# Optimization experiments

Hardware: AMD Instinct MI355X
Metric: run time of the kernel (lower is better)

Reference implementation:

```python
import jax, jax.numpy as jnp
import numpy as np

H, B, S, D, T = 4, 16, 2048, 128, 5  # n_head, batch, seq_len, d_model, num event types
BAND_K = 64  # latest-k band width, as in get_latest_k_mask


def setup_inputs() -> dict:
    key = jax.random.key(0)
    ks = jax.random.split(key, 5)
    output = jax.random.normal(ks[0], (B, S, D), dtype=jnp.float32)
    # banded 'latest-k' mask: mask[i, i:i+k] = 1  (start=max(i,i-k+1)=i, end=min(S,i+k))
    i = jnp.arange(S)
    band = ((i[None, :] >= i[:, None]) & (i[None, :] < i[:, None] + BAND_K)).astype(jnp.float32)
    local_cor = band[None]  # [1, S, S]
    cor_matrix = jax.random.normal(ks[1], (T, D), dtype=jnp.float32)
    event_type = jax.random.randint(ks[2], (B, S), 1, T + 1)  # 1-based event ids in [1, T]
    # per-head linear3 params (xavier-ish); self.linear is unused in forward
    W3 = jax.random.normal(ks[3], (H, D, D), dtype=jnp.float32) / np.sqrt(D)
    b3 = jnp.zeros((H, D), dtype=jnp.float32)
    return dict(output=output, local_cor=local_cor, cor_matrix=cor_matrix,
                event_type=event_type, W3=W3, b3=b3)


def reference(output, local_cor, cor_matrix, event_type, W3, b3):
    # (corr^T @ cor_matrix[et-1]).mean(2) == einsum('bsd,bs->bd', corr, cor_matrix[et-1].mean(-1))
    g = cor_matrix.mean(-1)[event_type - 1]  # [B, S]
    x = output
    sum_seq = jnp.zeros_like(output)          # sum over heads of [B,S,D]
    sum_head = jnp.zeros((output.shape[0], output.shape[2]), output.dtype)  # [B,D]
    for h in range(H):
        z = jax.nn.elu(jnp.einsum('bsd,ed->bse', x, W3[h]) + b3[h])  # linear3 + ELU
        corr = jnp.matmul(local_cor, z)       # [1,S,S] @ [B,S,D] -> [B,S,D]
        head_out = jnp.einsum('bsd,bs->bd', corr, g)  # [B,D]
        sum_seq = sum_seq + corr
        sum_head = sum_head + head_out
        x = corr                               # next head consumes correlation_output
    return (sum_seq, sum_head)
```

## Files before the change

kernel.cpp:

```cpp
#include <hip/hip_runtime.h>
#include <math.h>

#define NHEAD 4
#define BATCH 16
#define SEQ   2048
#define DMODEL 128
#define NTYPES 5
#define BAND  64
#define MROWS (BATCH * SEQ)

typedef __attribute__((ext_vector_type(8))) short bf16x8;
typedef __attribute__((ext_vector_type(4))) float f32x4;
typedef __attribute__((ext_vector_type(4))) unsigned int u32x4;

static __device__ __forceinline__ unsigned short f2bf(float f) {
  unsigned int u = __float_as_uint(f);
  unsigned int r = (u + 0x7fffu + ((u >> 16) & 1u)) >> 16;
  return (unsigned short)r;
}
static __device__ __forceinline__ float bflo(unsigned int v) {
  return __uint_as_float(v << 16);
}
static __device__ __forceinline__ float bfhi(unsigned int v) {
  return __uint_as_float(v & 0xffff0000u);
}
static __device__ __forceinline__ unsigned int pkbf(float lo, float hi) {
  return ((unsigned int)f2bf(hi) << 16) | (unsigned int)f2bf(lo);
}
static __device__ __forceinline__ int xcd_swz(int blk, int nwg) {
  return (blk & 7) * (nwg >> 3) + (blk >> 3);
}

__global__ __launch_bounds__(256) void init_kernel(
    const float* __restrict__ corm,
    const int* __restrict__ et,
    const float* __restrict__ W3,
    unsigned short* __restrict__ wbf,
    float* __restrict__ gbuf,
    float* __restrict__ sum_head) {
  __shared__ float rowmean[NTYPES];
  const int tid = threadIdx.x;
  const long t = (long)blockIdx.x * 256 + tid;

  if (t < (NHEAD * DMODEL * DMODEL) / 8) {
    const long u = t * 8;
    float4 a = *reinterpret_cast<const float4*>(W3 + u);
    float4 b = *reinterpret_cast<const float4*>(W3 + u + 4);
    unsigned short o[8];
    o[0] = f2bf(a.x); o[1] = f2bf(a.y); o[2] = f2bf(a.z); o[3] = f2bf(a.w);
    o[4] = f2bf(b.x); o[5] = f2bf(b.y); o[6] = f2bf(b.z); o[7] = f2bf(b.w);
    *reinterpret_cast<u32x4*>(wbf + u) = *reinterpret_cast<u32x4*>(o);
  }
  if (tid < NTYPES) {
    float s = 0.f;
    for (int d = 0; d < DMODEL; ++d) s += corm[tid * DMODEL + d];
    rowmean[tid] = s * (1.0f / DMODEL);
  }
  __syncthreads();
  if (t < MROWS) gbuf[t] = rowmean[et[t] - 1];
  if (t < BATCH * DMODEL) sum_head[t] = 0.f;
}

__global__ __launch_bounds__(512, 4) void gemm0_kernel(
    const float* __restrict__ X0,
    const unsigned short* __restrict__ Wb,
    const float* __restrict__ bvec,
    unsigned short* __restrict__ Zb) {
  __shared__ __align__(16) char lds[64 * 272 + 128 * 272];
  char* Xl = lds;
  char* Wl = lds + 64 * 272;
  const int tid = threadIdx.x;
  const int swz = xcd_swz(blockIdx.x, gridDim.x);
  const int row0 = swz * 64;

  #pragma unroll
  for (int it = 0; it < 2; ++it) {
    const int u = it * 512 + tid;
    const int r = u >> 4, g4 = u & 15;
    const float* xs = X0 + (long)(row0 + r) * DMODEL + g4 * 8;
    float4 f0 = *reinterpret_cast<const float4*>(xs);
    float4 f1 = *reinterpret_cast<const float4*>(xs + 4);
    unsigned short o[8];
    o[0] = f2bf(f0.x); o[1] = f2bf(f0.y); o[2] = f2bf(f0.z); o[3] = f2bf(f0.w);
    o[4] = f2bf(f1.x); o[5] = f2bf(f1.y); o[6] = f2bf(f1.z); o[7] = f2bf(f1.w);
    *reinterpret_cast<u32x4*>(Xl + r * 272 + g4 * 16) = *reinterpret_cast<u32x4*>(o);
  }
  #pragma unroll
  for (int it = 0; it < 4; ++it) {
    const int u = it * 512 + tid;
    const int e = u >> 4, g4 = u & 15;
    u32x4 v = *reinterpret_cast<const u32x4*>(Wb + e * DMODEL + g4 * 8);
    *reinterpret_cast<u32x4*>(Wl + e * 272 + g4 * 16) = v;
  }
  __syncthreads();

  const int wv = tid >> 6, l = tid & 63;
  const int mv = wv >> 1, nh = wv & 1;
  const int lr = l & 15, lk = l >> 4;
  f32x4 acc[4];
  #pragma unroll
  for (int n = 0; n < 4; ++n) acc[n] = (f32x4){0.f, 0.f, 0.f, 0.f};
  #pragma unroll
  for (int t = 0; t < 4; ++t) {
    const bf16x8 a = *reinterpret_cast<const bf16x8*>(
        Xl + (mv * 16 + lr) * 272 + (t * 4 + lk) * 16);
    #pragma unroll
    for (int n = 0; n < 4; ++n) {
      const bf16x8 bfrag = *reinterpret_cast<const bf16x8*>(
          Wl + (nh * 64 + n * 16 + lr) * 272 + (t * 4 + lk) * 16);
      acc[n] = __builtin_amdgcn_mfma_f32_16x16x32_bf16(a, bfrag, acc[n], 0, 0, 0);
    }
  }
  #pragma unroll
  for (int n = 0; n < 4; ++n) {
    const int col = nh * 64 + n * 16 + lr;
    const float bias = bvec[col];
    #pragma unroll
    for (int r = 0; r < 4; ++r) {
      const int row = row0 + mv * 16 + lk * 4 + r;
      float v = acc[n][r] + bias;
      const float e = expm1f(fminf(v, 0.f));
      v = v > 0.f ? v : e;
      Zb[(long)row * DMODEL + col] = f2bf(v);
    }
  }
}

template <int ACC>
__global__ __launch_bounds__(512, 4) void fused_band_gemm(
    const unsigned short* __restrict__ Zin,
    const unsigned short* __restrict__ CSin,
    unsigned short* __restrict__ Cout,
    const unsigned short* __restrict__ Wb,
    const float* __restrict__ bvec,
    unsigned short* __restrict__ Zout,
    float* __restrict__ SH,
    const float* __restrict__ Gbuf) {
  __shared__ __align__(16) char lds[56320];
  char* Xl = lds;
  float2* s8 = reinterpret_cast<float2*>(lds);
  unsigned int* zl = reinterpret_cast<unsigned int*>(lds + 17408);
  char* Wl = lds + 17408;
  float* hred = reinterpret_cast<float*>(lds + 52224);

  const int tid = threadIdx.x;
  const int swz = xcd_swz(blockIdx.x, gridDim.x);
  const int r0 = swz * 64;
  const int b = r0 >> 11, s0 = r0 & 2047;

  const unsigned int* zsrc = reinterpret_cast<const unsigned int*>(Zin) +
                             (long)b * SEQ * 64;
  #pragma unroll
  for (int it = 0; it < 4; ++it) {
    const int u = it * 512 + tid;
    const int r = u >> 4, c4 = u & 15;
    const int s = s0 + r;
    u32x4 v = (u32x4){0u, 0u, 0u, 0u};
    if (s < SEQ) v = *reinterpret_cast<const u32x4*>(zsrc + (long)s * 64 + c4 * 4);
    *reinterpret_cast<u32x4*>(zl + r * 64 + c4 * 4) = v;
  }

  const int p = tid & 63, q = tid >> 6;

  unsigned int csr[8];
  if (ACC) {
    #pragma unroll
    for (int i = 0; i < 8; ++i)
      csr[i] = *reinterpret_cast<const unsigned int*>(
          CSin + ((long)r0 + q * 8 + i) * DMODEL + 2 * p);
  }
  __syncthreads();

  #pragma unroll
  for (int j = 0; j < 2; ++j) {
    const int k = q * 2 + j;
    float a0 = 0.f, a1 = 0.f;
    #pragma unroll
    for (int jr = 0; jr < 8; ++jr) {
      const unsigned int v = zl[(k * 8 + jr) * 64 + p];
      a0 += bflo(v); a1 += bfhi(v);
    }
    s8[k * 64 + p] = make_float2(a0, a1);
  }
  __syncthreads();

  float w0 = 0.f, w1 = 0.f;
  #pragma unroll
  for (int j = 0; j < 8; ++j) {
    const float2 v = s8[(q + j) * 64 + p];
    w0 += v.x; w1 += v.y;
  }
  __syncthreads();

  float hs0 = 0.f, hs1 = 0.f;
  const float* gr = Gbuf + (long)b * SEQ + s0;
  #pragma unroll
  for (int i = 0; i < 8; ++i) {
    const int s = q * 8 + i;
    const float c0v = w0, c1v = w1;
    const float g = gr[s];
    hs0 += c0v * g; hs1 += c1v * g;
    unsigned int pk;
    if (ACC)
      pk = pkbf(c0v + bflo(csr[i]), c1v + bfhi(csr[i]));
    else
      pk = pkbf(c0v, c1v);
    *reinterpret_cast<unsigned int*>(
        Cout + ((long)r0 + s) * DMODEL + 2 * p) = pk;
    *reinterpret_cast<unsigned int*>(Xl + s * 272 + p * 4) =
        ACC ? pkbf(c0v, c1v) : pk;
    const unsigned int va = zl[(s + BAND) * 64 + p];
    const unsigned int vs = zl[s * 64 + p];
    w0 += bflo(va) - bflo(vs);
    w1 += bfhi(va) - bfhi(vs);
  }
  *reinterpret_cast<float2*>(hred + (p * 8 + q) * 2) = make_float2(hs0, hs1);
  __syncthreads();

  if (q == 0) {
    float t0 = 0.f, t1 = 0.f;
    #pragma unroll
    for (int k = 0; k < 8; ++k) {
      const float2 v = *reinterpret_cast<const float2*>(hred + (p * 8 + k) * 2);
      t0 += v.x; t1 += v.y;
    }
    atomicAdd(SH + b * DMODEL + 2 * p, t0);
    atomicAdd(SH + b * DMODEL + 2 * p + 1, t1);
  }
  #pragma unroll
  for (int it = 0; it < 4; ++it) {
    const int u = it * 512 + tid;
    const int e = u >> 4, g4 = u & 15;
    u32x4 v = *reinterpret_cast<const u32x4*>(Wb + e * DMODEL + g4 * 8);
    *reinterpret_cast<u32x4*>(Wl + e * 272 + g4 * 16) = v;
  }
  __syncthreads();

  const int wv = tid >> 6, l = tid & 63;
  const int mv = wv >> 1, nh = wv & 1;
  const int lr = l & 15, lk = l >> 4;
  f32x4 acc[4];
  #pragma unroll
  for (int n = 0; n < 4; ++n) acc[n] = (f32x4){0.f, 0.f, 0.f, 0.f};
  #pragma unroll
  for (int t = 0; t < 4; ++t) {
    const bf16x8 a = *reinterpret_cast<const bf16x8*>(
        Xl + (mv * 16 + lr) * 272 + (t * 4 + lk) * 16);
    #pragma unroll
    for (int n = 0; n < 4; ++n) {
      const bf16x8 bfrag = *reinterpret_cast<const bf16x8*>(
          Wl + (nh * 64 + n * 16 + lr) * 272 + (t * 4 + lk) * 16);
      acc[n] = __builtin_amdgcn_mfma_f32_16x16x32_bf16(a, bfrag, acc[n], 0, 0, 0);
    }
  }
  #pragma unroll
  for (int n = 0; n < 4; ++n) {
    const int col = nh * 64 + n * 16 + lr;
    const float bias = bvec[col];
    #pragma unroll
    for (int r = 0; r < 4; ++r) {
      const int row = r0 + mv * 16 + lk * 4 + r;
      float v = acc[n][r] + bias;
      const float e = expm1f(fminf(v, 0.f));
      v = v > 0.f ? v : e;
      Zout[(long)row * DMODEL + col] = f2bf(v);
    }
  }
}

__global__ __launch_bounds__(512, 4) void band3_kernel(
    const unsigned short* __restrict__ Zin,
    const unsigned short* __restrict__ CSin,
    float* __restrict__ SS,
    float* __restrict__ SH,
    const float* __restrict__ Gbuf) {
  __shared__ __align__(16) char lds[45056];
  unsigned int* zl = reinterpret_cast<unsigned int*>(lds);
  float2* s8 = reinterpret_cast<float2*>(lds + 32768);
  float* hred = reinterpret_cast<float*>(lds + 40960);

  const int tid = threadIdx.x;
  const int swz = xcd_swz(blockIdx.x, gridDim.x);
  const int r0 = swz * 64;
  const int b = r0 >> 11, s0 = r0 & 2047;

  const unsigned int* zsrc = reinterpret_cast<const unsigned int*>(Zin) +
                             (long)b * SEQ * 64;
  #pragma unroll
  for (int it = 0; it < 4; ++it) {
    const int u = it * 512 + tid;
    const int r = u >> 4, c4 = u & 15;
    const int s = s0 + r;
    u32x4 v = (u32x4){0u, 0u, 0u, 0u};
    if (s < SEQ) v = *reinterpret_cast<const u32x4*>(zsrc + (long)s * 64 + c4 * 4);
    *reinterpret_cast<u32x4*>(zl + r * 64 + c4 * 4) = v;
  }

  const int p = tid & 63, q = tid >> 6;
  unsigned int csr[8];
  #pragma unroll
  for (int i = 0; i < 8; ++i)
    csr[i] = *reinterpret_cast<const unsigned int*>(
        CSin + ((long)r0 + q * 8 + i) * DMODEL + 2 * p);
  __syncthreads();

  #pragma unroll
  for (int j = 0; j < 2; ++j) {
    const int k = q * 2 + j;
    float a0 = 0.f, a1 = 0.f;
    #pragma unroll
    for (int jr = 0; jr < 8; ++jr) {
      const unsigned int v = zl[(k * 8 + jr) * 64 + p];
      a0 += bflo(v); a1 += bfhi(v);
    }
    s8[k * 64 + p] = make_float2(a0, a1);
  }
  __syncthreads();

  float w0 = 0.f, w1 = 0.f;
  #pragma unroll
  for (int j = 0; j < 8; ++j) {
    const float2 v = s8[(q + j) * 64 + p];
    w0 += v.x; w1 += v.y;
  }
  float hs0 = 0.f, hs1 = 0.f;
  const float* gr = Gbuf + (long)b * SEQ + s0;
  #pragma unroll
  for (int i = 0; i < 8; ++i) {
    const int s = q * 8 + i;
    const float c0v = w0, c1v = w1;
    const float g = gr[s];
    hs0 += c0v * g; hs1 += c1v * g;
    const long orow = ((long)r0 + s) * DMODEL + 2 * p;
    float2 o;
    o.x = c0v + bflo(csr[i]);
    o.y = c1v + bfhi(csr[i]);
    *reinterpret_cast<float2*>(SS + orow) = o;
    const unsigned int va = zl[(s + BAND) * 64 + p];
    const unsigned int vs = zl[s * 64 + p];
    w0 += bflo(va) - bflo(vs);
    w1 += bfhi(va) - bfhi(vs);
  }
  *reinterpret_cast<float2*>(hred + (p * 8 + q) * 2) = make_float2(hs0, hs1);
  __syncthreads();
  if (q == 0) {
    float t0 = 0.f, t1 = 0.f;
    #pragma unroll
    for (int k = 0; k < 8; ++k) {
      const float2 v = *reinterpret_cast<const float2*>(hred + (p * 8 + k) * 2);
      t0 += v.x; t1 += v.y;
    }
    atomicAdd(SH + b * DMODEL + 2 * p, t0);
    atomicAdd(SH + b * DMODEL + 2 * p + 1, t1);
  }
}

extern "C" void kernel_launch(void* const* d_in, const int* in_sizes, int n_in,
                              void* d_out, int out_size, void* d_ws, size_t ws_size,
                              hipStream_t stream) {
  const float* x0   = (const float*)d_in[0];
  const float* corm = (const float*)d_in[2];
  const int*   et   = (const int*)d_in[3];
  const float* W3   = (const float*)d_in[4];
  const float* b3   = (const float*)d_in[5];

  float* out_ss = (float*)d_out;
  float* out_sh = out_ss + (size_t)MROWS * DMODEL;

  char* ws = (char*)d_ws;
  const size_t MB = 1024 * 1024;
  unsigned short* A = (unsigned short*)(ws + 0 * MB);
  unsigned short* B = (unsigned short*)(ws + 8 * MB);
  unsigned short* C = (unsigned short*)(ws + 16 * MB);
  unsigned short* D = (unsigned short*)(ws + 24 * MB);
  unsigned short* E = (unsigned short*)(ws + 32 * MB);
  unsigned short* wbf  = (unsigned short*)(ws + 40 * MB);
  float*          gbuf = (float*)(ws + 40 * MB + 131072);

  const size_t WSTR = (size_t)DMODEL * DMODEL;

  init_kernel<<<128, 256, 0, stream>>>(corm, et, W3, wbf, gbuf, out_sh);
  gemm0_kernel<<<512, 512, 0, stream>>>(x0, wbf, b3, A);
  fused_band_gemm<0><<<512, 512, 0, stream>>>(
      A, nullptr, B, wbf + 1 * WSTR, b3 + 1 * DMODEL, E, out_sh, gbuf);
  fused_band_gemm<1><<<512, 512, 0, stream>>>(
      E, B, C, wbf + 2 * WSTR, b3 + 2 * DMODEL, A, out_sh, gbuf);
  fused_band_gemm<1><<<512, 512, 0, stream>>>(
      A, C, D, wbf + 3 * WSTR, b3 + 3 * DMODEL, E, out_sh, gbuf);
  band3_kernel<<<512, 512, 0, stream>>>(E, D, out_ss, out_sh, gbuf);
}
```

Baseline: 63.17 us.

## Drop init kernel and fuse last band-gemm stage with final band pass

Removes the separate init kernel. Weight bf16 conversion, the event-type gate lookup and the zeroing of sum_head now happen inside the consuming kernels. The last fused band-GEMM and the final band kernel are merged into one 1024-thread block kernel. That block computes the head-2 band sum, the head-3 GEMM+ELU in LDS and the head-3 band sum, and writes the fp32 outputs directly, so the D/E intermediate round trips and two launches go away. In exchange, every block redundantly converts weights and recomputes row means, and the new kernel uses about 140KB of LDS, which limits occupancy to one block per CU.

```diff
diff --git a/kernel.cpp b/kernel.cpp
--- a/kernel.cpp
+++ b/kernel.cpp
@@ -31,47 +31,20 @@
   return (blk & 7) * (nwg >> 3) + (blk >> 3);
 }
 
-__global__ __launch_bounds__(256) void init_kernel(
-    const float* __restrict__ corm,
-    const int* __restrict__ et,
-    const float* __restrict__ W3,
-    unsigned short* __restrict__ wbf,
-    float* __restrict__ gbuf,
-    float* __restrict__ sum_head) {
-  __shared__ float rowmean[NTYPES];
-  const int tid = threadIdx.x;
-  const long t = (long)blockIdx.x * 256 + tid;
-
-  if (t < (NHEAD * DMODEL * DMODEL) / 8) {
-    const long u = t * 8;
-    float4 a = *reinterpret_cast<const float4*>(W3 + u);
-    float4 b = *reinterpret_cast<const float4*>(W3 + u + 4);
-    unsigned short o[8];
-    o[0] = f2bf(a.x); o[1] = f2bf(a.y); o[2] = f2bf(a.z); o[3] = f2bf(a.w);
-    o[4] = f2bf(b.x); o[5] = f2bf(b.y); o[6] = f2bf(b.z); o[7] = f2bf(b.w);
-    *reinterpret_cast<u32x4*>(wbf + u) = *reinterpret_cast<u32x4*>(o);
-  }
-  if (tid < NTYPES) {
-    float s = 0.f;
-    for (int d = 0; d < DMODEL; ++d) s += corm[tid * DMODEL + d];
-    rowmean[tid] = s * (1.0f / DMODEL);
-  }
-  __syncthreads();
-  if (t < MROWS) gbuf[t] = rowmean[et[t] - 1];
-  if (t < BATCH * DMODEL) sum_head[t] = 0.f;
-}
-
 __global__ __launch_bounds__(512, 4) void gemm0_kernel(
     const float* __restrict__ X0,
-    const unsigned short* __restrict__ Wb,
+    const float* __restrict__ W3h,
     const float* __restrict__ bvec,
-    unsigned short* __restrict__ Zb) {
+    unsigned short* __restrict__ Zb,
+    float* __restrict__ SH) {
   __shared__ __align__(16) char lds[64 * 272 + 128 * 272];
   char* Xl = lds;
   char* Wl = lds + 64 * 272;
   const int tid = threadIdx.x;
   const int swz = xcd_swz(blockIdx.x, gridDim.x);
   const int row0 = swz * 64;
+
+  if (blockIdx.x < 16 && tid < DMODEL) SH[blockIdx.x * DMODEL + tid] = 0.f;
 
   #pragma unroll
   for (int it = 0; it < 2; ++it) {
@@ -89,8 +62,13 @@
   for (int it = 0; it < 4; ++it) {
     const int u = it * 512 + tid;
     const int e = u >> 4, g4 = u & 15;
-    u32x4 v = *reinterpret_cast<const u32x4*>(Wb + e * DMODEL + g4 * 8);
-    *reinterpret_cast<u32x4*>(Wl + e * 272 + g4 * 16) = v;
+    const float* wsrc = W3h + e * DMODEL + g4 * 8;
+    float4 f0 = *reinterpret_cast<const float4*>(wsrc);
+    float4 f1 = *reinterpret_cast<const float4*>(wsrc + 4);
+    unsigned short o[8];
+    o[0] = f2bf(f0.x); o[1] = f2bf(f0.y); o[2] = f2bf(f0.z); o[3] = f2bf(f0.w);
+    o[4] = f2bf(f1.x); o[5] = f2bf(f1.y); o[6] = f2bf(f1.z); o[7] = f2bf(f1.w);
+    *reinterpret_cast<u32x4*>(Wl + e * 272 + g4 * 16) = *reinterpret_cast<u32x4*>(o);
   }
   __syncthreads();
 
@@ -131,12 +109,15 @@
     const unsigned short* __restrict__ Zin,
     const unsigned short* __restrict__ CSin,
     unsigned short* __restrict__ Cout,
-    const unsigned short* __restrict__ Wb,
+    const float* __restrict__ W3h,
     const float* __restrict__ bvec,
     unsigned short* __restrict__ Zout,
     float* __restrict__ SH,
-    const float* __restrict__ Gbuf) {
+    const int* __restrict__ et,
+    const float* __restrict__ corm) {
   __shared__ __align__(16) char lds[56320];
+  __shared__ float g_lds[64];
+  __shared__ float rowmean[NTYPES];
   char* Xl = lds;
   float2* s8 = reinterpret_cast<float2*>(lds);
   unsigned int* zl = reinterpret_cast<unsigned int*>(lds + 17408);
@@ -159,9 +140,12 @@
     if (s < SEQ) v = *reinterpret_cast<const u32x4*>(zsrc + (long)s * 64 + c4 * 4);
     *reinterpret_cast<u32x4*>(zl + r * 64 + c4 * 4) = v;
   }
-
+  if (tid < NTYPES) {
+    float s = 0.f;
+    for (int d = 0; d < DMODEL; ++d) s += corm[tid * DMODEL + d];
+    rowmean[tid] = s * (1.0f / DMODEL);
+  }
   const int p = tid & 63, q = tid >> 6;
-
   unsigned int csr[8];
   if (ACC) {
     #pragma unroll
@@ -171,6 +155,7 @@
   }
   __syncthreads();
 
+  if (tid < 64) g_lds[tid] = rowmean[et[(long)b * SEQ + s0 + tid] - 1];
   #pragma unroll
   for (int j = 0; j < 2; ++j) {
     const int k = q * 2 + j;
@@ -193,20 +178,18 @@
   __syncthreads();
 
   float hs0 = 0.f, hs1 = 0.f;
-  const float* gr = Gbuf + (long)b * SEQ + s0;
   #pragma unroll
   for (int i = 0; i < 8; ++i) {
     const int s = q * 8 + i;
     const float c0v = w0, c1v = w1;
-    const float g = gr[s];
+    const float g = g_lds[s];
     hs0 += c0v * g; hs1 += c1v * g;
     unsigned int pk;
     if (ACC)
       pk = pkbf(c0v + bflo(csr[i]), c1v + bfhi(csr[i]));
     else
       pk = pkbf(c0v, c1v);
-    *reinterpret_cast<unsigned int*>(
-        Cout + ((long)r0 + s) * DMODEL + 2 * p) = pk;
+    *reinterpret_cast<unsigned int*>(Cout + ((long)r0 + s) * DMODEL + 2 * p) = pk;
     *reinterpret_cast<unsigned int*>(Xl + s * 272 + p * 4) =
         ACC ? pkbf(c0v, c1v) : pk;
     const unsigned int va = zl[(s + BAND) * 64 + p];
@@ -231,8 +214,13 @@
   for (int it = 0; it < 4; ++it) {
     const int u = it * 512 + tid;
     const int e = u >> 4, g4 = u & 15;
-    u32x4 v = *reinterpret_cast<const u32x4*>(Wb + e * DMODEL + g4 * 8);
-    *reinterpret_cast<u32x4*>(Wl + e * 272 + g4 * 16) = v;
+    const float* wsrc = W3h + e * DMODEL + g4 * 8;
+    float4 f0 = *reinterpret_cast<const float4*>(wsrc);
+    float4 f1 = *reinterpret_cast<const float4*>(wsrc + 4);
+    unsigned short o[8];
+    o[0] = f2bf(f0.x); o[1] = f2bf(f0.y); o[2] = f2bf(f0.z); o[3] = f2bf(f0.w);
+    o[4] = f2bf(f1.x); o[5] = f2bf(f1.y); o[6] = f2bf(f1.z); o[7] = f2bf(f1.w);
+    *reinterpret_cast<u32x4*>(Wl + e * 272 + g4 * 16) = *reinterpret_cast<u32x4*>(o);
   }
   __syncthreads();
 
@@ -268,52 +256,85 @@
   }
 }
 
-__global__ __launch_bounds__(512, 4) void band3_kernel(
+__global__ __launch_bounds__(1024) void f2final_kernel(
     const unsigned short* __restrict__ Zin,
     const unsigned short* __restrict__ CSin,
+    const float* __restrict__ W3h,
+    const float* __restrict__ bvec,
     float* __restrict__ SS,
     float* __restrict__ SH,
-    const float* __restrict__ Gbuf) {
-  __shared__ __align__(16) char lds[45056];
-  unsigned int* zl = reinterpret_cast<unsigned int*>(lds);
-  float2* s8 = reinterpret_cast<float2*>(lds + 32768);
-  float* hred = reinterpret_cast<float*>(lds + 40960);
+    const int* __restrict__ et,
+    const float* __restrict__ corm) {
+  __shared__ __align__(16) char lds[140032];
+  __shared__ float g_lds[64];
+  __shared__ float rowmean[NTYPES];
+  unsigned int* zst = reinterpret_cast<unsigned int*>(lds);
+  char* Xl = lds + 49920;
+  char* Wl = lds + 84736;
+  float2* s8 = reinterpret_cast<float2*>(lds + 119552);
+  float* hred = reinterpret_cast<float*>(lds + 131840);
 
   const int tid = threadIdx.x;
   const int swz = xcd_swz(blockIdx.x, gridDim.x);
   const int r0 = swz * 64;
   const int b = r0 >> 11, s0 = r0 & 2047;
+  const int p = tid & 63, q = tid >> 6;
 
   const unsigned int* zsrc = reinterpret_cast<const unsigned int*>(Zin) +
                              (long)b * SEQ * 64;
   #pragma unroll
-  for (int it = 0; it < 4; ++it) {
-    const int u = it * 512 + tid;
+  for (int it = 0; it < 3; ++it) {
+    const int u = it * 1024 + tid;
     const int r = u >> 4, c4 = u & 15;
     const int s = s0 + r;
     u32x4 v = (u32x4){0u, 0u, 0u, 0u};
     if (s < SEQ) v = *reinterpret_cast<const u32x4*>(zsrc + (long)s * 64 + c4 * 4);
-    *reinterpret_cast<u32x4*>(zl + r * 64 + c4 * 4) = v;
-  }
-
-  const int p = tid & 63, q = tid >> 6;
+    *reinterpret_cast<u32x4*>(zst + r * 65 + c4 * 4) = v;
+  }
+  #pragma unroll
+  for (int it = 0; it < 2; ++it) {
+    const int u = it * 1024 + tid;
+    const int e = u >> 4, g4 = u & 15;
+    const float* wsrc = W3h + e * DMODEL + g4 * 8;
+    float4 f0 = *reinterpret_cast<const float4*>(wsrc);
+    float4 f1 = *reinterpret_cast<const float4*>(wsrc + 4);
+    unsigned short o[8];
+    o[0] = f2bf(f0.x); o[1] = f2bf(f0.y); o[2] = f2bf(f0.z); o[3] = f2bf(f0.w);
+    o[4] = f2bf(f1.x); o[5] = f2bf(f1.y); o[6] = f2bf(f1.z); o[7] = f2bf(f1.w);
+    *reinterpret_cast<u32x4*>(Wl + e * 272 + g4 * 16) = *reinterpret_cast<u32x4*>(o);
+  }
+  if (tid < NTYPES) {
+    float s = 0.f;
+    for (int d = 0; d < DMODEL; ++d) s += corm[tid * DMODEL + d];
+    rowmean[tid] = s * (1.0f / DMODEL);
+  }
   unsigned int csr[8];
-  #pragma unroll
-  for (int i = 0; i < 8; ++i)
-    csr[i] = *reinterpret_cast<const unsigned int*>(
-        CSin + ((long)r0 + q * 8 + i) * DMODEL + 2 * p);
-  __syncthreads();
-
-  #pragma unroll
-  for (int j = 0; j < 2; ++j) {
-    const int k = q * 2 + j;
+  if (q < 8) {
+    #pragma unroll
+    for (int i = 0; i < 8; ++i)
+      csr[i] = *reinterpret_cast<const unsigned int*>(
+          CSin + ((long)r0 + q * 8 + i) * DMODEL + 2 * p);
+  }
+  __syncthreads();
+
+  if (tid < 64) g_lds[tid] = rowmean[et[(long)b * SEQ + s0 + tid] - 1];
+  {
     float a0 = 0.f, a1 = 0.f;
     #pragma unroll
     for (int jr = 0; jr < 8; ++jr) {
-      const unsigned int v = zl[(k * 8 + jr) * 64 + p];
+      const unsigned int v = zst[(q * 8 + jr) * 65 + p];
       a0 += bflo(v); a1 += bfhi(v);
     }
-    s8[k * 64 + p] = make_float2(a0, a1);
+    s8[q * 64 + p] = make_float2(a0, a1);
+    if (q < 8) {
+      float b0 = 0.f, b1 = 0.f;
+      #pragma unroll
+      for (int jr = 0; jr < 8; ++jr) {
+        const unsigned int v = zst[((16 + q) * 8 + jr) * 65 + p];
+        b0 += bflo(v); b1 += bfhi(v);
+      }
+      s8[(16 + q) * 64 + p] = make_float2(b0, b1);
+    }
   }
   __syncthreads();
 
@@ -324,30 +345,103 @@
     w0 += v.x; w1 += v.y;
   }
   float hs0 = 0.f, hs1 = 0.f;
-  const float* gr = Gbuf + (long)b * SEQ + s0;
   #pragma unroll
   for (int i = 0; i < 8; ++i) {
     const int s = q * 8 + i;
     const float c0v = w0, c1v = w1;
-    const float g = gr[s];
-    hs0 += c0v * g; hs1 += c1v * g;
-    const long orow = ((long)r0 + s) * DMODEL + 2 * p;
-    float2 o;
-    o.x = c0v + bflo(csr[i]);
-    o.y = c1v + bfhi(csr[i]);
-    *reinterpret_cast<float2*>(SS + orow) = o;
-    const unsigned int va = zl[(s + BAND) * 64 + p];
-    const unsigned int vs = zl[s * 64 + p];
+    if (q < 8) {
+      const float g = g_lds[s];
+      hs0 += c0v * g; hs1 += c1v * g;
+    }
+    *reinterpret_cast<unsigned int*>(Xl + s * 272 + p * 4) = pkbf(c0v, c1v);
+    const unsigned int va = zst[(s + BAND) * 65 + p];
+    const unsigned int vs = zst[s * 65 + p];
     w0 += bflo(va) - bflo(vs);
     w1 += bfhi(va) - bfhi(vs);
   }
-  *reinterpret_cast<float2*>(hred + (p * 8 + q) * 2) = make_float2(hs0, hs1);
+  __syncthreads();
+
+  {
+    const int l = tid & 63;
+    const int mv = q >> 1, nh = q & 1;
+    const int lr = l & 15, lk = l >> 4;
+    f32x4 acc[4];
+    #pragma unroll
+    for (int n = 0; n < 4; ++n) acc[n] = (f32x4){0.f, 0.f, 0.f, 0.f};
+    #pragma unroll
+    for (int t = 0; t < 4; ++t) {
+      const bf16x8 a = *reinterpret_cast<const bf16x8*>(
+          Xl + (mv * 16 + lr) * 272 + (t * 4 + lk) * 16);
+      #pragma unroll
+      for (int n = 0; n < 4; ++n) {
+        const bf16x8 bfrag = *reinterpret_cast<const bf16x8*>(
+            Wl + (nh * 64 + n * 16 + lr) * 272 + (t * 4 + lk) * 16);
+        acc[n] = __builtin_amdgcn_mfma_f32_16x16x32_bf16(a, bfrag, acc[n], 0, 0, 0);
+      }
+    }
+    #pragma unroll
+    for (int n = 0; n < 4; ++n) {
+      const int col = nh * 64 + n * 16 + lr;
+      const float bias = bvec[col];
+      #pragma unroll
+      for (int r = 0; r < 4; ++r) {
+        const int row = mv * 16 + lk * 4 + r;
+        float v = acc[n][r] + bias;
+        const float e = expm1f(fminf(v, 0.f));
+        v = v > 0.f ? v : e;
+        const unsigned short bz =
+            (s0 + row < SEQ) ? f2bf(v) : (unsigned short)0;
+        *reinterpret_cast<unsigned short*>(
+            reinterpret_cast<char*>(zst) + row * 260 + col * 2) = bz;
+      }
+    }
+  }
+  __syncthreads();
+
+  {
+    float a0 = 0.f, a1 = 0.f;
+    #pragma unroll
+    for (int jr = 0; jr < 8; ++jr) {
+      const unsigned int v = zst[(q * 8 + jr) * 65 + p];
+      a0 += bflo(v); a1 += bfhi(v);
+    }
+    s8[q * 64 + p] = make_float2(a0, a1);
+  }
+  __syncthreads();
+
+  if (q < 8) {
+    float v0 = 0.f, v1 = 0.f;
+    #pragma unroll
+    for (int j = 0; j < 8; ++j) {
+      const float2 v = s8[(q + j) * 64 + p];
+      v0 += v.x; v1 += v.y;
+    }
+    #pragma unroll
+    for (int i = 0; i < 8; ++i) {
+      const int s = q * 8 + i;
+      const float c3l = v0, c3h = v1;
+      const float g = g_lds[s];
+      hs0 += c3l * g; hs1 += c3h * g;
+      const unsigned int c2 =
+          *reinterpret_cast<const unsigned int*>(Xl + s * 272 + p * 4);
+      float2 o;
+      o.x = c3l + bflo(c2) + bflo(csr[i]);
+      o.y = c3h + bfhi(c2) + bfhi(csr[i]);
+      *reinterpret_cast<float2*>(SS + ((long)r0 + s) * DMODEL + 2 * p) = o;
+      const unsigned int va = zst[(s + BAND) * 65 + p];
+      const unsigned int vs = zst[s * 65 + p];
+      v0 += bflo(va) - bflo(vs);
+      v1 += bfhi(va) - bfhi(vs);
+    }
+  }
+
+  *reinterpret_cast<float2*>(hred + (p * 16 + q) * 2) = make_float2(hs0, hs1);
   __syncthreads();
   if (q == 0) {
     float t0 = 0.f, t1 = 0.f;
     #pragma unroll
-    for (int k = 0; k < 8; ++k) {
-      const float2 v = *reinterpret_cast<const float2*>(hred + (p * 8 + k) * 2);
+    for (int k = 0; k < 16; ++k) {
+      const float2 v = *reinterpret_cast<const float2*>(hred + (p * 16 + k) * 2);
       t0 += v.x; t1 += v.y;
     }
     atomicAdd(SH + b * DMODEL + 2 * p, t0);
@@ -372,20 +466,15 @@
   unsigned short* A = (unsigned short*)(ws + 0 * MB);
   unsigned short* B = (unsigned short*)(ws + 8 * MB);
   unsigned short* C = (unsigned short*)(ws + 16 * MB);
-  unsigned short* D = (unsigned short*)(ws + 24 * MB);
-  unsigned short* E = (unsigned short*)(ws + 32 * MB);
-  unsigned short* wbf  = (unsigned short*)(ws + 40 * MB);
-  float*          gbuf = (float*)(ws + 40 * MB + 131072);
+  unsigned short* E = (unsigned short*)(ws + 24 * MB);
 
   const size_t WSTR = (size_t)DMODEL * DMODEL;
 
-  init_kernel<<<128, 256, 0, stream>>>(corm, et, W3, wbf, gbuf, out_sh);
-  gemm0_kernel<<<512, 512, 0, stream>>>(x0, wbf, b3, A);
+  gemm0_kernel<<<512, 512, 0, stream>>>(x0, W3, b3, A, out_sh);
   fused_band_gemm<0><<<512, 512, 0, stream>>>(
-      A, nullptr, B, wbf + 1 * WSTR, b3 + 1 * DMODEL, E, out_sh, gbuf);
+      A, nullptr, B, W3 + 1 * WSTR, b3 + 1 * DMODEL, E, out_sh, et, corm);
   fused_band_gemm<1><<<512, 512, 0, stream>>>(
-      E, B, C, wbf + 2 * WSTR, b3 + 2 * DMODEL, A, out_sh, gbuf);
-  fused_band_gemm<1><<<512, 512, 0, stream>>>(
-      A, C, D, wbf + 3 * WSTR, b3 + 3 * DMODEL, E, out_sh, gbuf);
-  band3_kernel<<<512, 512, 0, stream>>>(E, D, out_ss, out_sh, gbuf);
-}
+      E, B, C, W3 + 2 * WSTR, b3 + 2 * DMODEL, A, out_sh, et, corm);
+  f2final_kernel<<<512, 1024, 0, stream>>>(
+      A, C, W3 + 3 * WSTR, b3 + 3 * DMODEL, out_ss, out_sh, et, corm);
+}
```

New measurement: 65.19 us. 3.2% more time.

## Eliminate init kernel by fusing weight conversion, g computation into band kernels

Applied to the files above, without the earlier changes.

Removes the separate init kernel: W3 fp32->bf16 conversion is done inside each GEMM/band kernel, the per-type row means and g values are computed per block from corm and event_type, and sum_head zeroing moves into gemm0. The band kernels also stop staging Z through LDS and instead load the two needed rows per thread (s and s+64) directly into registers, prefetching W early to overlap with the window sums. This saves one launch and a global round-trip, at the cost of redundant conversion and reduction work in each of the 512 blocks and more register pressure.

```diff
diff --git a/kernel.cpp b/kernel.cpp
--- a/kernel.cpp
+++ b/kernel.cpp
@@ -31,47 +31,20 @@
   return (blk & 7) * (nwg >> 3) + (blk >> 3);
 }
 
-__global__ __launch_bounds__(256) void init_kernel(
-    const float* __restrict__ corm,
-    const int* __restrict__ et,
-    const float* __restrict__ W3,
-    unsigned short* __restrict__ wbf,
-    float* __restrict__ gbuf,
-    float* __restrict__ sum_head) {
-  __shared__ float rowmean[NTYPES];
-  const int tid = threadIdx.x;
-  const long t = (long)blockIdx.x * 256 + tid;
-
-  if (t < (NHEAD * DMODEL * DMODEL) / 8) {
-    const long u = t * 8;
-    float4 a = *reinterpret_cast<const float4*>(W3 + u);
-    float4 b = *reinterpret_cast<const float4*>(W3 + u + 4);
-    unsigned short o[8];
-    o[0] = f2bf(a.x); o[1] = f2bf(a.y); o[2] = f2bf(a.z); o[3] = f2bf(a.w);
-    o[4] = f2bf(b.x); o[5] = f2bf(b.y); o[6] = f2bf(b.z); o[7] = f2bf(b.w);
-    *reinterpret_cast<u32x4*>(wbf + u) = *reinterpret_cast<u32x4*>(o);
-  }
-  if (tid < NTYPES) {
-    float s = 0.f;
-    for (int d = 0; d < DMODEL; ++d) s += corm[tid * DMODEL + d];
-    rowmean[tid] = s * (1.0f / DMODEL);
-  }
-  __syncthreads();
-  if (t < MROWS) gbuf[t] = rowmean[et[t] - 1];
-  if (t < BATCH * DMODEL) sum_head[t] = 0.f;
-}
-
 __global__ __launch_bounds__(512, 4) void gemm0_kernel(
     const float* __restrict__ X0,
-    const unsigned short* __restrict__ Wb,
+    const float* __restrict__ W3h,
     const float* __restrict__ bvec,
-    unsigned short* __restrict__ Zb) {
+    unsigned short* __restrict__ Zb,
+    float* __restrict__ SH) {
   __shared__ __align__(16) char lds[64 * 272 + 128 * 272];
   char* Xl = lds;
   char* Wl = lds + 64 * 272;
   const int tid = threadIdx.x;
   const int swz = xcd_swz(blockIdx.x, gridDim.x);
   const int row0 = swz * 64;
+
+  if (blockIdx.x < 16 && tid < DMODEL) SH[blockIdx.x * DMODEL + tid] = 0.f;
 
   #pragma unroll
   for (int it = 0; it < 2; ++it) {
@@ -89,8 +62,13 @@
   for (int it = 0; it < 4; ++it) {
     const int u = it * 512 + tid;
     const int e = u >> 4, g4 = u & 15;
-    u32x4 v = *reinterpret_cast<const u32x4*>(Wb + e * DMODEL + g4 * 8);
-    *reinterpret_cast<u32x4*>(Wl + e * 272 + g4 * 16) = v;
+    const float* wsrc = W3h + e * DMODEL + g4 * 8;
+    float4 f0 = *reinterpret_cast<const float4*>(wsrc);
+    float4 f1 = *reinterpret_cast<const float4*>(wsrc + 4);
+    unsigned short o[8];
+    o[0] = f2bf(f0.x); o[1] = f2bf(f0.y); o[2] = f2bf(f0.z); o[3] = f2bf(f0.w);
+    o[4] = f2bf(f1.x); o[5] = f2bf(f1.y); o[6] = f2bf(f1.z); o[7] = f2bf(f1.w);
+    *reinterpret_cast<u32x4*>(Wl + e * 272 + g4 * 16) = *reinterpret_cast<u32x4*>(o);
   }
   __syncthreads();
 
@@ -131,37 +109,36 @@
     const unsigned short* __restrict__ Zin,
     const unsigned short* __restrict__ CSin,
     unsigned short* __restrict__ Cout,
-    const unsigned short* __restrict__ Wb,
+    const float* __restrict__ W3h,
     const float* __restrict__ bvec,
     unsigned short* __restrict__ Zout,
     float* __restrict__ SH,
-    const float* __restrict__ Gbuf) {
+    const int* __restrict__ et,
+    const float* __restrict__ corm) {
   __shared__ __align__(16) char lds[56320];
+  __shared__ float g_lds[64];
+  __shared__ float rowmean[NTYPES];
   char* Xl = lds;
-  float2* s8 = reinterpret_cast<float2*>(lds);
-  unsigned int* zl = reinterpret_cast<unsigned int*>(lds + 17408);
   char* Wl = lds + 17408;
+  float2* s8 = reinterpret_cast<float2*>(lds + 17408);
   float* hred = reinterpret_cast<float*>(lds + 52224);
 
   const int tid = threadIdx.x;
   const int swz = xcd_swz(blockIdx.x, gridDim.x);
   const int r0 = swz * 64;
   const int b = r0 >> 11, s0 = r0 & 2047;
-
-  const unsigned int* zsrc = reinterpret_cast<const unsigned int*>(Zin) +
-                             (long)b * SEQ * 64;
-  #pragma unroll
-  for (int it = 0; it < 4; ++it) {
-    const int u = it * 512 + tid;
-    const int r = u >> 4, c4 = u & 15;
-    const int s = s0 + r;
-    u32x4 v = (u32x4){0u, 0u, 0u, 0u};
-    if (s < SEQ) v = *reinterpret_cast<const u32x4*>(zsrc + (long)s * 64 + c4 * 4);
-    *reinterpret_cast<u32x4*>(zl + r * 64 + c4 * 4) = v;
-  }
-
   const int p = tid & 63, q = tid >> 6;
 
+  const unsigned int* zsrc =
+      reinterpret_cast<const unsigned int*>(Zin) + (long)b * SEQ * 64 + p;
+  unsigned int zlo[8], zhi[8];
+  #pragma unroll
+  for (int i = 0; i < 8; ++i) {
+    const int sl = s0 + q * 8 + i;
+    zlo[i] = zsrc[(long)sl * 64];
+    const int sh_ = sl + BAND;
+    zhi[i] = (sh_ < SEQ) ? zsrc[(long)sh_ * 64] : 0u;
+  }
   unsigned int csr[8];
   if (ACC) {
     #pragma unroll
@@ -169,18 +146,40 @@
       csr[i] = *reinterpret_cast<const unsigned int*>(
           CSin + ((long)r0 + q * 8 + i) * DMODEL + 2 * p);
   }
-  __syncthreads();
-
-  #pragma unroll
-  for (int j = 0; j < 2; ++j) {
-    const int k = q * 2 + j;
-    float a0 = 0.f, a1 = 0.f;
-    #pragma unroll
-    for (int jr = 0; jr < 8; ++jr) {
-      const unsigned int v = zl[(k * 8 + jr) * 64 + p];
-      a0 += bflo(v); a1 += bfhi(v);
-    }
-    s8[k * 64 + p] = make_float2(a0, a1);
+  u32x4 wfr[4];
+  #pragma unroll
+  for (int it = 0; it < 4; ++it) {
+    const int u = it * 512 + tid;
+    const int e = u >> 4, g4 = u & 15;
+    const float* wsrc = W3h + e * DMODEL + g4 * 8;
+    float4 f0 = *reinterpret_cast<const float4*>(wsrc);
+    float4 f1 = *reinterpret_cast<const float4*>(wsrc + 4);
+    unsigned short o[8];
+    o[0] = f2bf(f0.x); o[1] = f2bf(f0.y); o[2] = f2bf(f0.z); o[3] = f2bf(f0.w);
+    o[4] = f2bf(f1.x); o[5] = f2bf(f1.y); o[6] = f2bf(f1.z); o[7] = f2bf(f1.w);
+    wfr[it] = *reinterpret_cast<u32x4*>(o);
+  }
+  int etv = 1;
+  if (tid < 64) etv = et[(long)b * SEQ + s0 + tid];
+  if (tid < 64) {
+    #pragma unroll
+    for (int t = 0; t < NTYPES; ++t) {
+      float v = corm[t * DMODEL + tid] + corm[t * DMODEL + 64 + tid];
+      #pragma unroll
+      for (int o = 32; o > 0; o >>= 1) v += __shfl_xor(v, o, 64);
+      if (tid == 0) rowmean[t] = v * (1.0f / DMODEL);
+    }
+  }
+
+  {
+    float a0 = 0.f, a1 = 0.f, b0 = 0.f, b1 = 0.f;
+    #pragma unroll
+    for (int i = 0; i < 8; ++i) {
+      a0 += bflo(zlo[i]); a1 += bfhi(zlo[i]);
+      b0 += bflo(zhi[i]); b1 += bfhi(zhi[i]);
+    }
+    s8[q * 64 + p] = make_float2(a0, a1);
+    s8[(q + 8) * 64 + p] = make_float2(b0, b1);
   }
   __syncthreads();
 
@@ -190,29 +189,32 @@
     const float2 v = s8[(q + j) * 64 + p];
     w0 += v.x; w1 += v.y;
   }
-  __syncthreads();
-
+  if (tid < 64) g_lds[tid] = rowmean[etv - 1];
+  __syncthreads();
+
+  #pragma unroll
+  for (int it = 0; it < 4; ++it) {
+    const int u = it * 512 + tid;
+    const int e = u >> 4, g4 = u & 15;
+    *reinterpret_cast<u32x4*>(Wl + e * 272 + g4 * 16) = wfr[it];
+  }
   float hs0 = 0.f, hs1 = 0.f;
-  const float* gr = Gbuf + (long)b * SEQ + s0;
   #pragma unroll
   for (int i = 0; i < 8; ++i) {
     const int s = q * 8 + i;
     const float c0v = w0, c1v = w1;
-    const float g = gr[s];
+    const float g = g_lds[s];
     hs0 += c0v * g; hs1 += c1v * g;
     unsigned int pk;
     if (ACC)
       pk = pkbf(c0v + bflo(csr[i]), c1v + bfhi(csr[i]));
     else
       pk = pkbf(c0v, c1v);
-    *reinterpret_cast<unsigned int*>(
-        Cout + ((long)r0 + s) * DMODEL + 2 * p) = pk;
+    *reinterpret_cast<unsigned int*>(Cout + ((long)r0 + s) * DMODEL + 2 * p) = pk;
     *reinterpret_cast<unsigned int*>(Xl + s * 272 + p * 4) =
         ACC ? pkbf(c0v, c1v) : pk;
-    const unsigned int va = zl[(s + BAND) * 64 + p];
-    const unsigned int vs = zl[s * 64 + p];
-    w0 += bflo(va) - bflo(vs);
-    w1 += bfhi(va) - bfhi(vs);
+    w0 += bflo(zhi[i]) - bflo(zlo[i]);
+    w1 += bfhi(zhi[i]) - bfhi(zlo[i]);
   }
   *reinterpret_cast<float2*>(hred + (p * 8 + q) * 2) = make_float2(hs0, hs1);
   __syncthreads();
@@ -227,15 +229,6 @@
     atomicAdd(SH + b * DMODEL + 2 * p, t0);
     atomicAdd(SH + b * DMODEL + 2 * p + 1, t1);
   }
-  #pragma unroll
-  for (int it = 0; it < 4; ++it) {
-    const int u = it * 512 + tid;
-    const int e = u >> 4, g4 = u & 15;
-    u32x4 v = *reinterpret_cast<const u32x4*>(Wb + e * DMODEL + g4 * 8);
-    *reinterpret_cast<u32x4*>(Wl + e * 272 + g4 * 16) = v;
-  }
-  __syncthreads();
-
   const int wv = tid >> 6, l = tid & 63;
   const int mv = wv >> 1, nh = wv & 1;
   const int lr = l & 15, lk = l >> 4;
@@ -273,47 +266,51 @@
     const unsigned short* __restrict__ CSin,
     float* __restrict__ SS,
     float* __restrict__ SH,
-    const float* __restrict__ Gbuf) {
-  __shared__ __align__(16) char lds[45056];
-  unsigned int* zl = reinterpret_cast<unsigned int*>(lds);
-  float2* s8 = reinterpret_cast<float2*>(lds + 32768);
-  float* hred = reinterpret_cast<float*>(lds + 40960);
+    const int* __restrict__ et,
+    const float* __restrict__ corm) {
+  __shared__ float2 s8[16 * 64];
+  __shared__ float hred[64 * 8 * 2];
+  __shared__ float g_lds[64];
+  __shared__ float rowmean[NTYPES];
 
   const int tid = threadIdx.x;
   const int swz = xcd_swz(blockIdx.x, gridDim.x);
   const int r0 = swz * 64;
   const int b = r0 >> 11, s0 = r0 & 2047;
-
-  const unsigned int* zsrc = reinterpret_cast<const unsigned int*>(Zin) +
-                             (long)b * SEQ * 64;
-  #pragma unroll
-  for (int it = 0; it < 4; ++it) {
-    const int u = it * 512 + tid;
-    const int r = u >> 4, c4 = u & 15;
-    const int s = s0 + r;
-    u32x4 v = (u32x4){0u, 0u, 0u, 0u};
-    if (s < SEQ) v = *reinterpret_cast<const u32x4*>(zsrc + (long)s * 64 + c4 * 4);
-    *reinterpret_cast<u32x4*>(zl + r * 64 + c4 * 4) = v;
-  }
-
   const int p = tid & 63, q = tid >> 6;
-  unsigned int csr[8];
-  #pragma unroll
-  for (int i = 0; i < 8; ++i)
+
+  const unsigned int* zsrc =
+      reinterpret_cast<const unsigned int*>(Zin) + (long)b * SEQ * 64 + p;
+  unsigned int zlo[8], zhi[8], csr[8];
+  #pragma unroll
+  for (int i = 0; i < 8; ++i) {
+    const int sl = s0 + q * 8 + i;
+    zlo[i] = zsrc[(long)sl * 64];
+    const int sh_ = sl + BAND;
+    zhi[i] = (sh_ < SEQ) ? zsrc[(long)sh_ * 64] : 0u;
     csr[i] = *reinterpret_cast<const unsigned int*>(
         CSin + ((long)r0 + q * 8 + i) * DMODEL + 2 * p);
-  __syncthreads();
-
-  #pragma unroll
-  for (int j = 0; j < 2; ++j) {
-    const int k = q * 2 + j;
-    float a0 = 0.f, a1 = 0.f;
-    #pragma unroll
-    for (int jr = 0; jr < 8; ++jr) {
-      const unsigned int v = zl[(k * 8 + jr) * 64 + p];
-      a0 += bflo(v); a1 += bfhi(v);
-    }
-    s8[k * 64 + p] = make_float2(a0, a1);
+  }
+  int etv = 1;
+  if (tid < 64) etv = et[(long)b * SEQ + s0 + tid];
+  if (tid < 64) {
+    #pragma unroll
+    for (int t = 0; t < NTYPES; ++t) {
+      float v = corm[t * DMODEL + tid] + corm[t * DMODEL + 64 + tid];
+      #pragma unroll
+      for (int o = 32; o > 0; o >>= 1) v += __shfl_xor(v, o, 64);
+      if (tid == 0) rowmean[t] = v * (1.0f / DMODEL);
+    }
+  }
+  {
+    float a0 = 0.f, a1 = 0.f, b0 = 0.f, b1 = 0.f;
+    #pragma unroll
+    for (int i = 0; i < 8; ++i) {
+      a0 += bflo(zlo[i]); a1 += bfhi(zlo[i]);
+      b0 += bflo(zhi[i]); b1 += bfhi(zhi[i]);
+    }
+    s8[q * 64 + p] = make_float2(a0, a1);
+    s8[(q + 8) * 64 + p] = make_float2(b0, b1);
   }
   __syncthreads();
 
@@ -323,23 +320,22 @@
     const float2 v = s8[(q + j) * 64 + p];
     w0 += v.x; w1 += v.y;
   }
+  if (tid < 64) g_lds[tid] = rowmean[etv - 1];
+  __syncthreads();
+
   float hs0 = 0.f, hs1 = 0.f;
-  const float* gr = Gbuf + (long)b * SEQ + s0;
   #pragma unroll
   for (int i = 0; i < 8; ++i) {
     const int s = q * 8 + i;
     const float c0v = w0, c1v = w1;
-    const float g = gr[s];
+    const float g = g_lds[s];
     hs0 += c0v * g; hs1 += c1v * g;
-    const long orow = ((long)r0 + s) * DMODEL + 2 * p;
     float2 o;
     o.x = c0v + bflo(csr[i]);
     o.y = c1v + bfhi(csr[i]);
-    *reinterpret_cast<float2*>(SS + orow) = o;
-    const unsigned int va = zl[(s + BAND) * 64 + p];
-    const unsigned int vs = zl[s * 64 + p];
-    w0 += bflo(va) - bflo(vs);
-    w1 += bfhi(va) - bfhi(vs);
+    *reinterpret_cast<float2*>(SS + ((long)r0 + s) * DMODEL + 2 * p) = o;
+    w0 += bflo(zhi[i]) - bflo(zlo[i]);
+    w1 += bfhi(zhi[i]) - bfhi(zlo[i]);
   }
   *reinterpret_cast<float2*>(hred + (p * 8 + q) * 2) = make_float2(hs0, hs1);
   __syncthreads();
@@ -374,18 +370,15 @@
   unsigned short* C = (unsigned short*)(ws + 16 * MB);
   unsigned short* D = (unsigned short*)(ws + 24 * MB);
   unsigned short* E = (unsigned short*)(ws + 32 * MB);
-  unsigned short* wbf  = (unsigned short*)(ws + 40 * MB);
-  float*          gbuf = (float*)(ws + 40 * MB + 131072);
 
   const size_t WSTR = (size_t)DMODEL * DMODEL;
 
-  init_kernel<<<128, 256, 0, stream>>>(corm, et, W3, wbf, gbuf, out_sh);
-  gemm0_kernel<<<512, 512, 0, stream>>>(x0, wbf, b3, A);
+  gemm0_kernel<<<512, 512, 0, stream>>>(x0, W3, b3, A, out_sh);
   fused_band_gemm<0><<<512, 512, 0, stream>>>(
-      A, nullptr, B, wbf + 1 * WSTR, b3 + 1 * DMODEL, E, out_sh, gbuf);
+      A, nullptr, B, W3 + 1 * WSTR, b3 + 1 * DMODEL, E, out_sh, et, corm);
   fused_band_gemm<1><<<512, 512, 0, stream>>>(
-      E, B, C, wbf + 2 * WSTR, b3 + 2 * DMODEL, A, out_sh, gbuf);
+      E, B, C, W3 + 2 * WSTR, b3 + 2 * DMODEL, A, out_sh, et, corm);
   fused_band_gemm<1><<<512, 512, 0, stream>>>(
-      A, C, D, wbf + 3 * WSTR, b3 + 3 * DMODEL, E, out_sh, gbuf);
-  band3_kernel<<<512, 512, 0, stream>>>(E, D, out_ss, out_sh, gbuf);
-}
+      A, C, D, W3 + 3 * WSTR, b3 + 3 * DMODEL, E, out_sh, et, corm);
+  band3_kernel<<<512, 512, 0, stream>>>(E, D, out_ss, out_sh, et, corm);
+}
```

After: 62.12 us. Within noise of the previous version (-1.7%).
